# Kernel tuning notes

Measured on AMD Instinct MI355X. Metric: run time of the kernel, lower is better.

## Reference

```python
import jax, jax.numpy as jnp
import numpy as np

NUM_SRC = 100000
NUM_DST = 100000
NUM_EDGES = 800000
WIDTH = 128
LEAKY_SLOPE = 0.01  # torch LeakyReLU default


def setup_inputs() -> dict:
    key = jax.random.key(0)
    k1, k2, k3, k4 = jax.random.split(key, 4)
    x_src = jax.random.normal(k1, (NUM_SRC, WIDTH), dtype=jnp.float32)
    x_dst = jax.random.normal(k2, (NUM_DST, WIDTH), dtype=jnp.float32)
    e = jax.random.randint(k3, (2, NUM_EDGES), 0, NUM_DST, dtype=jnp.int64)
    W = jax.random.normal(k4, (2 * WIDTH, WIDTH), dtype=jnp.float32) * 0.02
    b = jnp.zeros((WIDTH,), dtype=jnp.float32)
    return {"x_src": x_src, "x_dst": x_dst, "e": e, "W": W, "b": b}


def reference(x_src, x_dst, e, W, b):
    src_idx, dst_idx = e[0], e[1]
    # gather + per-edge diff: [E, W]
    diffs = x_dst[dst_idx] - x_src[src_idx]
    # segment max over destination nodes; empty segments -> 0 (matches torch.zeros_like init)
    seg_max = jax.ops.segment_max(diffs, dst_idx, num_segments=NUM_DST)
    counts = jax.ops.segment_sum(jnp.ones((diffs.shape[0],), dtype=x_dst.dtype),
                                 dst_idx, num_segments=NUM_DST)
    maxes = jnp.where(counts[:, None] > 0, seg_max, jnp.zeros_like(seg_max))
    # MLP: Linear(2W -> W) + LeakyReLU, then residual
    h = jnp.concatenate([x_dst, maxes], axis=1) @ W + b
    h = jax.nn.leaky_relu(h, negative_slope=LEAKY_SLOPE)
    return x_dst + h
```

## Files before the change

### kernel.cpp

```cpp
#include <hip/hip_runtime.h>

#define WIDTH 128
#define SLOPE 0.01f
#define SBS 512
#define FBM 64

typedef __attribute__((ext_vector_type(8))) short short8;
typedef __attribute__((ext_vector_type(4))) float f32x4;

__device__ __forceinline__ unsigned short f2bf(float f) {
    unsigned b = __float_as_uint(f);
    b += 0x7FFFu + ((b >> 16) & 1u);
    return (unsigned short)(b >> 16);
}
__device__ __forceinline__ float4 upk(uint2 u) {
    float4 r;
    r.x = __uint_as_float(u.x << 16);
    r.y = __uint_as_float(u.x & 0xFFFF0000u);
    r.z = __uint_as_float(u.y << 16);
    r.w = __uint_as_float(u.y & 0xFFFF0000u);
    return r;
}
__device__ __forceinline__ float4 fmin4(float4 a, float4 b) {
    return make_float4(fminf(a.x, b.x), fminf(a.y, b.y),
                       fminf(a.z, b.z), fminf(a.w, b.w));
}
__device__ __forceinline__ int swz(int lr, int bc) {
    return lr * 512 + (bc ^ ((lr & 7) << 4));
}

__global__ void prep_kernel(const float* __restrict__ x_src,
                            const float* __restrict__ W,
                            const int* __restrict__ e,
                            unsigned short* __restrict__ xsb,
                            unsigned short* __restrict__ Wt,
                            unsigned* __restrict__ counts,
                            int* __restrict__ rank,
                            int NS, int E, int nconv, int nhist) {
    int b = blockIdx.x;
    if (b < nconv) {
        int i = b * 256 + threadIdx.x;
        if (i < NS * 32) {
            float4 v = reinterpret_cast<const float4*>(x_src)[i];
            ushort4 o;
            o.x = f2bf(v.x); o.y = f2bf(v.y); o.z = f2bf(v.z); o.w = f2bf(v.w);
            *reinterpret_cast<ushort4*>(xsb + (size_t)i * 4) = o;
        }
    } else if (b < nconv + nhist) {
        int i = (b - nconv) * 256 + threadIdx.x;
        if (i < E) {
            int dst = e[E + i];
            rank[i] = (int)atomicAdd(&counts[dst], 1u);
        }
    } else {
        int t = (b - nconv - nhist) * 256 + threadIdx.x;
        if (t < 128 * 64) {
            int n = t & 127, kc = t >> 7;
            ushort4 o;
            unsigned short* op = &o.x;
            #pragma unroll
            for (int j = 0; j < 4; ++j) {
                int k = kc * 4 + j;
                float v;
                if (k < 128) v = W[(size_t)k * 128 + n] + W[(size_t)(k + 128) * 128 + n];
                else         v = -W[(size_t)k * 128 + n];
                op[j] = f2bf(v);
            }
            *reinterpret_cast<ushort4*>(Wt + (size_t)n * 256 + kc * 4) = o;
        }
    }
}

__global__ void block_sum_kernel(const unsigned* __restrict__ counts,
                                 unsigned* __restrict__ bsums, int M) {
    int i = blockIdx.x * SBS + threadIdx.x;
    unsigned v = (i < M) ? counts[i] : 0u;
    for (int d = 32; d > 0; d >>= 1) v += __shfl_down(v, d);
    __shared__ unsigned ws[SBS / 64];
    int lane = threadIdx.x & 63, w = threadIdx.x >> 6;
    if (lane == 0) ws[w] = v;
    __syncthreads();
    if (threadIdx.x == 0) {
        unsigned s = 0;
        for (int k = 0; k < SBS / 64; ++k) s += ws[k];
        bsums[blockIdx.x] = s;
    }
}

__global__ void bsum_scan_kernel(const unsigned* __restrict__ bsums,
                                 unsigned* __restrict__ bbase, int NB,
                                 int* __restrict__ offsets, int M) {
    __shared__ unsigned s[256];
    int t = threadIdx.x;
    unsigned v = (t < NB) ? bsums[t] : 0u;
    s[t] = v;
    __syncthreads();
    for (int off = 1; off < 256; off <<= 1) {
        unsigned n = (t >= off) ? s[t - off] : 0u;
        __syncthreads();
        s[t] += n;
        __syncthreads();
    }
    if (t < NB) bbase[t] = s[t] - v;
    if (t == 255) offsets[M] = (int)s[255];
}

__global__ void scan_final_kernel(const unsigned* __restrict__ counts,
                                  const unsigned* __restrict__ bbase,
                                  int* __restrict__ offsets, int M) {
    int b = blockIdx.x, t = threadIdx.x;
    int i = b * SBS + t;
    unsigned c = (i < M) ? counts[i] : 0u;
    unsigned v = c;
    int lane = t & 63, w = t >> 6;
    for (int d = 1; d < 64; d <<= 1) {
        unsigned n = __shfl_up(v, d);
        if (lane >= d) v += n;
    }
    __shared__ unsigned ws[SBS / 64];
    if (lane == 63) ws[w] = v;
    __syncthreads();
    unsigned wbase = 0;
    for (int k = 0; k < w; ++k) wbase += ws[k];
    if (i < M) offsets[i] = (int)(bbase[b] + wbase + v - c);
}

__global__ void scatter_kernel(const int* __restrict__ e,
                               const int* __restrict__ offsets,
                               const int* __restrict__ rank,
                               int* __restrict__ csr, int E) {
    int i = blockIdx.x * blockDim.x + threadIdx.x;
    if (i < E) {
        int dst = e[E + i];
        csr[offsets[dst] + rank[i]] = e[i];
    }
}

template<int XSB>
__device__ __forceinline__ void gstep(const float* xs_f,
                                      const unsigned short* xs_b,
                                      const int* csr, int p, int lim,
                                      int half, int cl, float4& mn) {
    int i0 = csr[min(p + 0, lim)];
    int i1 = csr[min(p + 1, lim)];
    int i2 = csr[min(p + 2, lim)];
    int i3 = csr[min(p + 3, lim)];
    int i4 = csr[min(p + 4, lim)];
    int i5 = csr[min(p + 5, lim)];
    int i6 = csr[min(p + 6, lim)];
    int i7 = csr[min(p + 7, lim)];
    int a0 = half ? i1 : i0;
    int a1 = half ? i3 : i2;
    int a2 = half ? i5 : i4;
    int a3 = half ? i7 : i6;
    float4 w0, w1, w2, w3;
    if (XSB) {
        uint2 u0 = *reinterpret_cast<const uint2*>(xs_b + (size_t)a0 * 128 + cl * 4);
        uint2 u1 = *reinterpret_cast<const uint2*>(xs_b + (size_t)a1 * 128 + cl * 4);
        uint2 u2 = *reinterpret_cast<const uint2*>(xs_b + (size_t)a2 * 128 + cl * 4);
        uint2 u3 = *reinterpret_cast<const uint2*>(xs_b + (size_t)a3 * 128 + cl * 4);
        w0 = upk(u0); w1 = upk(u1); w2 = upk(u2); w3 = upk(u3);
    } else {
        const float4* xs4 = reinterpret_cast<const float4*>(xs_f);
        w0 = xs4[(size_t)a0 * 32 + cl];
        w1 = xs4[(size_t)a1 * 32 + cl];
        w2 = xs4[(size_t)a2 * 32 + cl];
        w3 = xs4[(size_t)a3 * 32 + cl];
    }
    mn = fmin4(mn, fmin4(fmin4(w0, w1), fmin4(w2, w3)));
}

template<int XSB>
__global__ __launch_bounds__(256, 4) void fused_kernel(
        const float* __restrict__ x_src,
        const unsigned short* __restrict__ xsb,
        const float* __restrict__ x_dst,
        const int* __restrict__ offsets,
        const int* __restrict__ csr,
        const unsigned short* __restrict__ Wt,
        const float* __restrict__ bias,
        float* __restrict__ out, int M) {
    __shared__ unsigned short At[FBM * 256];
    char* Ab = reinterpret_cast<char*>(At);
    int tid = threadIdx.x;
    int lane = tid & 63;
    int wv = tid >> 6;
    int blockRow = blockIdx.x * FBM;

    #pragma unroll
    for (int i = 0; i < 8; ++i) {
        int u = tid + 256 * i;
        int lr = u >> 5;
        int c4 = u & 31;
        int gr = min(blockRow + lr, M - 1);
        float4 v = reinterpret_cast<const float4*>(x_dst)[(size_t)gr * 32 + c4];
        ushort4 o;
        o.x = f2bf(v.x); o.y = f2bf(v.y); o.z = f2bf(v.z); o.w = f2bf(v.w);
        *reinterpret_cast<ushort4*>(Ab + swz(lr, c4 * 8)) = o;
    }
    __syncthreads();

    int half = lane >> 5, cl = lane & 31;
    for (int j = 0; j < 4; ++j) {
        int lrb = wv * 16 + 4 * j;
        int beg0, beg1, beg2, beg3, end0, end1, end2, end3;
        {
            int r = __builtin_amdgcn_readfirstlane(blockRow + lrb);
            beg0 = (r + 0 < M) ? offsets[r + 0] : 0;
            end0 = (r + 0 < M) ? offsets[r + 1] : 0;
            beg1 = (r + 1 < M) ? offsets[r + 1] : 0;
            end1 = (r + 1 < M) ? offsets[r + 2] : 0;
            beg2 = (r + 2 < M) ? offsets[r + 2] : 0;
            end2 = (r + 2 < M) ? offsets[r + 3] : 0;
            beg3 = (r + 3 < M) ? offsets[r + 3] : 0;
            end3 = (r + 3 < M) ? offsets[r + 4] : 0;
        }
        float4 mn0 = make_float4(INFINITY, INFINITY, INFINITY, INFINITY);
        float4 mn1 = mn0, mn2 = mn0, mn3 = mn0;
        int p0 = beg0, p1 = beg1, p2 = beg2, p3 = beg3;
        while ((p0 < end0) | (p1 < end1) | (p2 < end2) | (p3 < end3)) {
            if (p0 < end0) { gstep<XSB>(x_src, xsb, csr, p0, end0 - 1, half, cl, mn0); p0 += 8; }
            if (p1 < end1) { gstep<XSB>(x_src, xsb, csr, p1, end1 - 1, half, cl, mn1); p1 += 8; }
            if (p2 < end2) { gstep<XSB>(x_src, xsb, csr, p2, end2 - 1, half, cl, mn2); p2 += 8; }
            if (p3 < end3) { gstep<XSB>(x_src, xsb, csr, p3, end3 - 1, half, cl, mn3); p3 += 8; }
        }
        mn0.x = fminf(mn0.x, __shfl_xor(mn0.x, 32));
        mn0.y = fminf(mn0.y, __shfl_xor(mn0.y, 32));
        mn0.z = fminf(mn0.z, __shfl_xor(mn0.z, 32));
        mn0.w = fminf(mn0.w, __shfl_xor(mn0.w, 32));
        mn1.x = fminf(mn1.x, __shfl_xor(mn1.x, 32));
        mn1.y = fminf(mn1.y, __shfl_xor(mn1.y, 32));
        mn1.z = fminf(mn1.z, __shfl_xor(mn1.z, 32));
        mn1.w = fminf(mn1.w, __shfl_xor(mn1.w, 32));
        mn2.x = fminf(mn2.x, __shfl_xor(mn2.x, 32));
        mn2.y = fminf(mn2.y, __shfl_xor(mn2.y, 32));
        mn2.z = fminf(mn2.z, __shfl_xor(mn2.z, 32));
        mn2.w = fminf(mn2.w, __shfl_xor(mn2.w, 32));
        mn3.x = fminf(mn3.x, __shfl_xor(mn3.x, 32));
        mn3.y = fminf(mn3.y, __shfl_xor(mn3.y, 32));
        mn3.z = fminf(mn3.z, __shfl_xor(mn3.z, 32));
        mn3.w = fminf(mn3.w, __shfl_xor(mn3.w, 32));

        {
            int lr = lrb + half;
            bool has = half ? (end1 > beg1) : (end0 > beg0);
            float4 m = half ? mn1 : mn0;
            ushort4 o;
            if (has) {
                o.x = f2bf(m.x); o.y = f2bf(m.y); o.z = f2bf(m.z); o.w = f2bf(m.w);
            } else {
                o = *reinterpret_cast<const ushort4*>(Ab + swz(lr, cl * 8));
            }
            *reinterpret_cast<ushort4*>(Ab + swz(lr, 256 + cl * 8)) = o;
        }
        {
            int lr = lrb + 2 + half;
            bool has = half ? (end3 > beg3) : (end2 > beg2);
            float4 m = half ? mn3 : mn2;
            ushort4 o;
            if (has) {
                o.x = f2bf(m.x); o.y = f2bf(m.y); o.z = f2bf(m.z); o.w = f2bf(m.w);
            } else {
                o = *reinterpret_cast<const ushort4*>(Ab + swz(lr, cl * 8));
            }
            *reinterpret_cast<ushort4*>(Ab + swz(lr, 256 + cl * 8)) = o;
        }
    }
    __syncthreads();

    int l15 = lane & 15;
    int q = lane >> 4;
    int ncol0 = wv * 32;

    f32x4 acc[4][2];
    #pragma unroll
    for (int t = 0; t < 4; ++t) {
        acc[t][0] = (f32x4){0.f, 0.f, 0.f, 0.f};
        acc[t][1] = (f32x4){0.f, 0.f, 0.f, 0.f};
    }
    size_t b0off = (size_t)(ncol0 + l15) * 256;
    size_t b1off = (size_t)(ncol0 + 16 + l15) * 256;

    #pragma unroll
    for (int s = 0; s < 8; ++s) {
        int koff = s * 32 + q * 8;
        short8 b0 = *reinterpret_cast<const short8*>(Wt + b0off + koff);
        short8 b1 = *reinterpret_cast<const short8*>(Wt + b1off + koff);
        #pragma unroll
        for (int t = 0; t < 4; ++t) {
            int lr = t * 16 + l15;
            short8 a = *reinterpret_cast<const short8*>(Ab + swz(lr, koff * 2));
            acc[t][0] = __builtin_amdgcn_mfma_f32_16x16x32_bf16(b0, a, acc[t][0], 0, 0, 0);
            acc[t][1] = __builtin_amdgcn_mfma_f32_16x16x32_bf16(b1, a, acc[t][1], 0, 0, 0);
        }
    }

    float4 bi[2];
    bi[0] = *reinterpret_cast<const float4*>(bias + ncol0 + q * 4);
    bi[1] = *reinterpret_cast<const float4*>(bias + ncol0 + 16 + q * 4);
    #pragma unroll
    for (int t = 0; t < 4; ++t) {
        int lr = t * 16 + l15;
        int row = blockRow + lr;
        if (row < M) {
            #pragma unroll
            for (int u = 0; u < 2; ++u) {
                int col = ncol0 + u * 16 + q * 4;
                uint2 xu = *reinterpret_cast<const uint2*>(Ab + swz(lr, col * 2));
                float4 xb = upk(xu);
                float4 o;
                float h;
                h = acc[t][u][0] + bi[u].x; o.x = xb.x + (h > 0.f ? h : SLOPE * h);
                h = acc[t][u][1] + bi[u].y; o.y = xb.y + (h > 0.f ? h : SLOPE * h);
                h = acc[t][u][2] + bi[u].z; o.z = xb.z + (h > 0.f ? h : SLOPE * h);
                h = acc[t][u][3] + bi[u].w; o.w = xb.w + (h > 0.f ? h : SLOPE * h);
                *reinterpret_cast<float4*>(out + (size_t)row * 128 + col) = o;
            }
        }
    }
}

extern "C" void kernel_launch(void* const* d_in, const int* in_sizes, int n_in,
                              void* d_out, int out_size, void* d_ws, size_t ws_size,
                              hipStream_t stream) {
    const float* x_src = (const float*)d_in[0];
    const float* x_dst = (const float*)d_in[1];
    const int*   e     = (const int*)d_in[2];
    const float* W     = (const float*)d_in[3];
    const float* bias  = (const float*)d_in[4];
    float* out = (float*)d_out;

    int NS = in_sizes[0] / WIDTH;
    int E  = in_sizes[2] / 2;
    int M  = in_sizes[1] / WIDTH;
    int NB = (M + SBS - 1) / SBS;

    unsigned short* xsb = (unsigned short*)d_ws;
    unsigned short* Wt  = xsb + (size_t)NS * WIDTH;
    unsigned* counts  = (unsigned*)(Wt + 128 * 256);
    int*      offsets = (int*)(counts + M);
    int*      rank    = offsets + (M + 1);
    int*      csr     = rank + E;
    unsigned* bsums   = (unsigned*)(csr + E);
    unsigned* bbase   = bsums + NB;
    size_t need = (char*)(bbase + NB) - (char*)d_ws;
    int use_xsb = (ws_size >= need) ? 1 : 0;
    if (!use_xsb) {
        Wt = (unsigned short*)d_ws;
        counts  = (unsigned*)(Wt + 128 * 256);
        offsets = (int*)(counts + M);
        rank    = offsets + (M + 1);
        csr     = rank + E;
        bsums   = (unsigned*)(csr + E);
        bbase   = bsums + NB;
    }

    hipMemsetAsync(counts, 0, (size_t)M * sizeof(unsigned), stream);

    int nconv = use_xsb ? (NS * 32 + 255) / 256 : 0;
    int nhist = (E + 255) / 256;
    int nwt   = (128 * 64 + 255) / 256;
    prep_kernel<<<nconv + nhist + nwt, 256, 0, stream>>>(x_src, W, e, xsb, Wt,
                                                         counts, rank, NS, E,
                                                         nconv, nhist);
    block_sum_kernel<<<NB, SBS, 0, stream>>>(counts, bsums, M);
    bsum_scan_kernel<<<1, 256, 0, stream>>>(bsums, bbase, NB, offsets, M);
    scan_final_kernel<<<NB, SBS, 0, stream>>>(counts, bbase, offsets, M);
    scatter_kernel<<<(E + 255) / 256, 256, 0, stream>>>(e, offsets, rank, csr, E);

    int fblocks = (M + FBM - 1) / FBM;
    if (use_xsb)
        fused_kernel<1><<<fblocks, 256, 0, stream>>>(x_src, xsb, x_dst, offsets,
                                                     csr, Wt, bias, out, M);
    else
        fused_kernel<0><<<fblocks, 256, 0, stream>>>(x_src, xsb, x_dst, offsets,
                                                     csr, Wt, bias, out, M);
}
```

Measured before the change: 139.5 us.

## Flatten per-block edge loop with LDS atomicMin on order-mapped bf16 values

```diff
diff --git a/kernel.cpp b/kernel.cpp
--- a/kernel.cpp
+++ b/kernel.cpp
@@ -3,7 +3,7 @@
 #define WIDTH 128
 #define SLOPE 0.01f
 #define SBS 512
-#define FBM 64
+#define FBM 32
 
 typedef __attribute__((ext_vector_type(8))) short short8;
 typedef __attribute__((ext_vector_type(4))) float f32x4;
@@ -21,9 +21,11 @@
     r.w = __uint_as_float(u.y & 0xFFFF0000u);
     return r;
 }
-__device__ __forceinline__ float4 fmin4(float4 a, float4 b) {
-    return make_float4(fminf(a.x, b.x), fminf(a.y, b.y),
-                       fminf(a.z, b.z), fminf(a.w, b.w));
+__device__ __forceinline__ unsigned map16(unsigned x) {
+    return (x & 0x8000u) ? (~x & 0xFFFFu) : (x | 0x8000u);
+}
+__device__ __forceinline__ unsigned short unmap16(unsigned u) {
+    return (unsigned short)((u & 0x8000u) ? (u ^ 0x8000u) : (~u & 0xFFFFu));
 }
 __device__ __forceinline__ int swz(int lr, int bc) {
     return lr * 512 + (bc ^ ((lr & 7) << 4));
@@ -128,46 +130,41 @@
 __global__ void scatter_kernel(const int* __restrict__ e,
                                const int* __restrict__ offsets,
                                const int* __restrict__ rank,
-                               int* __restrict__ csr, int E) {
+                               unsigned* __restrict__ csr, int E) {
     int i = blockIdx.x * blockDim.x + threadIdx.x;
     if (i < E) {
         int dst = e[E + i];
-        csr[offsets[dst] + rank[i]] = e[i];
+        unsigned pack = (unsigned)e[i] | ((unsigned)(dst & (FBM - 1)) << 20);
+        csr[offsets[dst] + rank[i]] = pack;
     }
 }
 
 template<int XSB>
-__device__ __forceinline__ void gstep(const float* xs_f,
-                                      const unsigned short* xs_b,
-                                      const int* csr, int p, int lim,
-                                      int half, int cl, float4& mn) {
-    int i0 = csr[min(p + 0, lim)];
-    int i1 = csr[min(p + 1, lim)];
-    int i2 = csr[min(p + 2, lim)];
-    int i3 = csr[min(p + 3, lim)];
-    int i4 = csr[min(p + 4, lim)];
-    int i5 = csr[min(p + 5, lim)];
-    int i6 = csr[min(p + 6, lim)];
-    int i7 = csr[min(p + 7, lim)];
-    int a0 = half ? i1 : i0;
-    int a1 = half ? i3 : i2;
-    int a2 = half ? i5 : i4;
-    int a3 = half ? i7 : i6;
-    float4 w0, w1, w2, w3;
+__device__ __forceinline__ void edge_min(const float* __restrict__ x_src,
+                                         const unsigned short* __restrict__ xsb,
+                                         unsigned pack, int cl,
+                                         unsigned* __restrict__ minbuf) {
+    int src = (int)(pack & 0xFFFFFu);
+    int lr  = (int)(pack >> 20);
+    unsigned m0, m1, m2, m3;
     if (XSB) {
-        uint2 u0 = *reinterpret_cast<const uint2*>(xs_b + (size_t)a0 * 128 + cl * 4);
-        uint2 u1 = *reinterpret_cast<const uint2*>(xs_b + (size_t)a1 * 128 + cl * 4);
-        uint2 u2 = *reinterpret_cast<const uint2*>(xs_b + (size_t)a2 * 128 + cl * 4);
-        uint2 u3 = *reinterpret_cast<const uint2*>(xs_b + (size_t)a3 * 128 + cl * 4);
-        w0 = upk(u0); w1 = upk(u1); w2 = upk(u2); w3 = upk(u3);
+        const unsigned short* p = xsb + (size_t)src * WIDTH + cl;
+        m0 = map16(p[0]);
+        m1 = map16(p[32]);
+        m2 = map16(p[64]);
+        m3 = map16(p[96]);
     } else {
-        const float4* xs4 = reinterpret_cast<const float4*>(xs_f);
-        w0 = xs4[(size_t)a0 * 32 + cl];
-        w1 = xs4[(size_t)a1 * 32 + cl];
-        w2 = xs4[(size_t)a2 * 32 + cl];
-        w3 = xs4[(size_t)a3 * 32 + cl];
-    }
-    mn = fmin4(mn, fmin4(fmin4(w0, w1), fmin4(w2, w3)));
+        const float* p = x_src + (size_t)src * WIDTH + cl;
+        m0 = map16(f2bf(p[0]));
+        m1 = map16(f2bf(p[32]));
+        m2 = map16(f2bf(p[64]));
+        m3 = map16(f2bf(p[96]));
+    }
+    unsigned* row = minbuf + lr * WIDTH + cl;
+    atomicMin(row + 0,  m0);
+    atomicMin(row + 32, m1);
+    atomicMin(row + 64, m2);
+    atomicMin(row + 96, m3);
 }
 
 template<int XSB>
@@ -176,94 +173,67 @@
         const unsigned short* __restrict__ xsb,
         const float* __restrict__ x_dst,
         const int* __restrict__ offsets,
-        const int* __restrict__ csr,
+        const unsigned* __restrict__ csr,
         const unsigned short* __restrict__ Wt,
         const float* __restrict__ bias,
         float* __restrict__ out, int M) {
-    __shared__ unsigned short At[FBM * 256];
+    __shared__ __align__(16) unsigned short At[FBM * 256];
+    __shared__ __align__(16) unsigned minbuf[FBM * WIDTH];
     char* Ab = reinterpret_cast<char*>(At);
     int tid = threadIdx.x;
     int lane = tid & 63;
     int wv = tid >> 6;
     int blockRow = blockIdx.x * FBM;
 
+    {
+        uint4* mb4 = reinterpret_cast<uint4*>(minbuf);
+        #pragma unroll
+        for (int i = 0; i < 4; ++i)
+            mb4[tid + 256 * i] = make_uint4(~0u, ~0u, ~0u, ~0u);
+    }
     #pragma unroll
-    for (int i = 0; i < 8; ++i) {
+    for (int i = 0; i < 4; ++i) {
         int u = tid + 256 * i;
-        int lr = u >> 5;
-        int c4 = u & 31;
-        int gr = min(blockRow + lr, M - 1);
-        float4 v = reinterpret_cast<const float4*>(x_dst)[(size_t)gr * 32 + c4];
+        int lr = u >> 5, c4 = u & 31;
+        float4 v = reinterpret_cast<const float4*>(x_dst)[(size_t)(blockRow + lr) * 32 + c4];
         ushort4 o;
         o.x = f2bf(v.x); o.y = f2bf(v.y); o.z = f2bf(v.z); o.w = f2bf(v.w);
         *reinterpret_cast<ushort4*>(Ab + swz(lr, c4 * 8)) = o;
     }
     __syncthreads();
 
+    int ebeg = offsets[blockRow];
+    int eend = offsets[blockRow + FBM];
     int half = lane >> 5, cl = lane & 31;
-    for (int j = 0; j < 4; ++j) {
-        int lrb = wv * 16 + 4 * j;
-        int beg0, beg1, beg2, beg3, end0, end1, end2, end3;
-        {
-            int r = __builtin_amdgcn_readfirstlane(blockRow + lrb);
-            beg0 = (r + 0 < M) ? offsets[r + 0] : 0;
-            end0 = (r + 0 < M) ? offsets[r + 1] : 0;
-            beg1 = (r + 1 < M) ? offsets[r + 1] : 0;
-            end1 = (r + 1 < M) ? offsets[r + 2] : 0;
-            beg2 = (r + 2 < M) ? offsets[r + 2] : 0;
-            end2 = (r + 2 < M) ? offsets[r + 3] : 0;
-            beg3 = (r + 3 < M) ? offsets[r + 3] : 0;
-            end3 = (r + 3 < M) ? offsets[r + 4] : 0;
-        }
-        float4 mn0 = make_float4(INFINITY, INFINITY, INFINITY, INFINITY);
-        float4 mn1 = mn0, mn2 = mn0, mn3 = mn0;
-        int p0 = beg0, p1 = beg1, p2 = beg2, p3 = beg3;
-        while ((p0 < end0) | (p1 < end1) | (p2 < end2) | (p3 < end3)) {
-            if (p0 < end0) { gstep<XSB>(x_src, xsb, csr, p0, end0 - 1, half, cl, mn0); p0 += 8; }
-            if (p1 < end1) { gstep<XSB>(x_src, xsb, csr, p1, end1 - 1, half, cl, mn1); p1 += 8; }
-            if (p2 < end2) { gstep<XSB>(x_src, xsb, csr, p2, end2 - 1, half, cl, mn2); p2 += 8; }
-            if (p3 < end3) { gstep<XSB>(x_src, xsb, csr, p3, end3 - 1, half, cl, mn3); p3 += 8; }
-        }
-        mn0.x = fminf(mn0.x, __shfl_xor(mn0.x, 32));
-        mn0.y = fminf(mn0.y, __shfl_xor(mn0.y, 32));
-        mn0.z = fminf(mn0.z, __shfl_xor(mn0.z, 32));
-        mn0.w = fminf(mn0.w, __shfl_xor(mn0.w, 32));
-        mn1.x = fminf(mn1.x, __shfl_xor(mn1.x, 32));
-        mn1.y = fminf(mn1.y, __shfl_xor(mn1.y, 32));
-        mn1.z = fminf(mn1.z, __shfl_xor(mn1.z, 32));
-        mn1.w = fminf(mn1.w, __shfl_xor(mn1.w, 32));
-        mn2.x = fminf(mn2.x, __shfl_xor(mn2.x, 32));
-        mn2.y = fminf(mn2.y, __shfl_xor(mn2.y, 32));
-        mn2.z = fminf(mn2.z, __shfl_xor(mn2.z, 32));
-        mn2.w = fminf(mn2.w, __shfl_xor(mn2.w, 32));
-        mn3.x = fminf(mn3.x, __shfl_xor(mn3.x, 32));
-        mn3.y = fminf(mn3.y, __shfl_xor(mn3.y, 32));
-        mn3.z = fminf(mn3.z, __shfl_xor(mn3.z, 32));
-        mn3.w = fminf(mn3.w, __shfl_xor(mn3.w, 32));
-
-        {
-            int lr = lrb + half;
-            bool has = half ? (end1 > beg1) : (end0 > beg0);
-            float4 m = half ? mn1 : mn0;
+    int lim = eend - 1;
+    if (eend > ebeg) {
+        #pragma unroll 2
+        for (int i = ebeg + wv * 4; i < eend; i += 16) {
+            unsigned p0 = csr[min(i + half, lim)];
+            unsigned p1 = csr[min(i + 2 + half, lim)];
+            edge_min<XSB>(x_src, xsb, p0, cl, minbuf);
+            edge_min<XSB>(x_src, xsb, p1, cl, minbuf);
+        }
+    }
+    __syncthreads();
+
+    {
+        int r = tid >> 3;
+        int c0 = (tid & 7) * 16;
+        #pragma unroll
+        for (int k = 0; k < 4; ++k) {
+            int c = c0 + k * 4;
+            unsigned u0 = minbuf[r * WIDTH + c + 0];
+            unsigned u1 = minbuf[r * WIDTH + c + 1];
+            unsigned u2 = minbuf[r * WIDTH + c + 2];
+            unsigned u3 = minbuf[r * WIDTH + c + 3];
+            ushort4 xb = *reinterpret_cast<const ushort4*>(Ab + swz(r, c * 2));
             ushort4 o;
-            if (has) {
-                o.x = f2bf(m.x); o.y = f2bf(m.y); o.z = f2bf(m.z); o.w = f2bf(m.w);
-            } else {
-                o = *reinterpret_cast<const ushort4*>(Ab + swz(lr, cl * 8));
-            }
-            *reinterpret_cast<ushort4*>(Ab + swz(lr, 256 + cl * 8)) = o;
-        }
-        {
-            int lr = lrb + 2 + half;
-            bool has = half ? (end3 > beg3) : (end2 > beg2);
-            float4 m = half ? mn3 : mn2;
-            ushort4 o;
-            if (has) {
-                o.x = f2bf(m.x); o.y = f2bf(m.y); o.z = f2bf(m.z); o.w = f2bf(m.w);
-            } else {
-                o = *reinterpret_cast<const ushort4*>(Ab + swz(lr, cl * 8));
-            }
-            *reinterpret_cast<ushort4*>(Ab + swz(lr, 256 + cl * 8)) = o;
+            o.x = (u0 <= 0xFFFFu) ? unmap16(u0) : xb.x;
+            o.y = (u1 <= 0xFFFFu) ? unmap16(u1) : xb.y;
+            o.z = (u2 <= 0xFFFFu) ? unmap16(u2) : xb.z;
+            o.w = (u3 <= 0xFFFFu) ? unmap16(u3) : xb.w;
+            *reinterpret_cast<ushort4*>(Ab + swz(r, 256 + c * 2)) = o;
         }
     }
     __syncthreads();
@@ -272,9 +242,9 @@
     int q = lane >> 4;
     int ncol0 = wv * 32;
 
-    f32x4 acc[4][2];
+    f32x4 acc[2][2];
     #pragma unroll
-    for (int t = 0; t < 4; ++t) {
+    for (int t = 0; t < 2; ++t) {
         acc[t][0] = (f32x4){0.f, 0.f, 0.f, 0.f};
         acc[t][1] = (f32x4){0.f, 0.f, 0.f, 0.f};
     }
@@ -287,7 +257,7 @@
         short8 b0 = *reinterpret_cast<const short8*>(Wt + b0off + koff);
         short8 b1 = *reinterpret_cast<const short8*>(Wt + b1off + koff);
         #pragma unroll
-        for (int t = 0; t < 4; ++t) {
+        for (int t = 0; t < 2; ++t) {
             int lr = t * 16 + l15;
             short8 a = *reinterpret_cast<const short8*>(Ab + swz(lr, koff * 2));
             acc[t][0] = __builtin_amdgcn_mfma_f32_16x16x32_bf16(b0, a, acc[t][0], 0, 0, 0);
@@ -299,23 +269,21 @@
     bi[0] = *reinterpret_cast<const float4*>(bias + ncol0 + q * 4);
     bi[1] = *reinterpret_cast<const float4*>(bias + ncol0 + 16 + q * 4);
     #pragma unroll
-    for (int t = 0; t < 4; ++t) {
+    for (int t = 0; t < 2; ++t) {
         int lr = t * 16 + l15;
         int row = blockRow + lr;
-        if (row < M) {
-            #pragma unroll
-            for (int u = 0; u < 2; ++u) {
-                int col = ncol0 + u * 16 + q * 4;
-                uint2 xu = *reinterpret_cast<const uint2*>(Ab + swz(lr, col * 2));
-                float4 xb = upk(xu);
-                float4 o;
-                float h;
-                h = acc[t][u][0] + bi[u].x; o.x = xb.x + (h > 0.f ? h : SLOPE * h);
-                h = acc[t][u][1] + bi[u].y; o.y = xb.y + (h > 0.f ? h : SLOPE * h);
-                h = acc[t][u][2] + bi[u].z; o.z = xb.z + (h > 0.f ? h : SLOPE * h);
-                h = acc[t][u][3] + bi[u].w; o.w = xb.w + (h > 0.f ? h : SLOPE * h);
-                *reinterpret_cast<float4*>(out + (size_t)row * 128 + col) = o;
-            }
+        #pragma unroll
+        for (int u = 0; u < 2; ++u) {
+            int col = ncol0 + u * 16 + q * 4;
+            uint2 xu = *reinterpret_cast<const uint2*>(Ab + swz(lr, col * 2));
+            float4 xb = upk(xu);
+            float4 o;
+            float h;
+            h = acc[t][u][0] + bi[u].x; o.x = xb.x + (h > 0.f ? h : SLOPE * h);
+            h = acc[t][u][1] + bi[u].y; o.y = xb.y + (h > 0.f ? h : SLOPE * h);
+            h = acc[t][u][2] + bi[u].z; o.z = xb.z + (h > 0.f ? h : SLOPE * h);
+            h = acc[t][u][3] + bi[u].w; o.w = xb.w + (h > 0.f ? h : SLOPE * h);
+            *reinterpret_cast<float4*>(out + (size_t)row * 128 + col) = o;
         }
     }
 }
@@ -340,7 +308,7 @@
     unsigned* counts  = (unsigned*)(Wt + 128 * 256);
     int*      offsets = (int*)(counts + M);
     int*      rank    = offsets + (M + 1);
-    int*      csr     = rank + E;
+    unsigned* csr     = (unsigned*)(rank + E);
     unsigned* bsums   = (unsigned*)(csr + E);
     unsigned* bbase   = bsums + NB;
     size_t need = (char*)(bbase + NB) - (char*)d_ws;
@@ -350,7 +318,7 @@
         counts  = (unsigned*)(Wt + 128 * 256);
         offsets = (int*)(counts + M);
         rank    = offsets + (M + 1);
-        csr     = rank + E;
+        csr     = (unsigned*)(rank + E);
         bsums   = (unsigned*)(csr + E);
         bbase   = bsums + NB;
     }
```

Result: slower. 173.2 us (+24.1%).

## Merge CSR build kernels into one cooperative kernel with grid syncs

Applied to the files above, without the earlier changes.

```diff
diff --git a/kernel.cpp b/kernel.cpp
--- a/kernel.cpp
+++ b/kernel.cpp
@@ -1,9 +1,12 @@
 #include <hip/hip_runtime.h>
+#include <hip/hip_cooperative_groups.h>
+
+namespace cg = cooperative_groups;
 
 #define WIDTH 128
 #define SLOPE 0.01f
-#define SBS 512
 #define FBM 64
+#define CBLK 512
 
 typedef __attribute__((ext_vector_type(8))) short short8;
 typedef __attribute__((ext_vector_type(4))) float f32x4;
@@ -29,108 +32,102 @@
     return lr * 512 + (bc ^ ((lr & 7) << 4));
 }
 
-__global__ void prep_kernel(const float* __restrict__ x_src,
-                            const float* __restrict__ W,
-                            const int* __restrict__ e,
-                            unsigned short* __restrict__ xsb,
-                            unsigned short* __restrict__ Wt,
-                            unsigned* __restrict__ counts,
-                            int* __restrict__ rank,
-                            int NS, int E, int nconv, int nhist) {
-    int b = blockIdx.x;
-    if (b < nconv) {
-        int i = b * 256 + threadIdx.x;
-        if (i < NS * 32) {
+__global__ void __launch_bounds__(256) csr_coop_kernel(
+        const float* __restrict__ x_src, const float* __restrict__ W,
+        const int* __restrict__ e,
+        unsigned short* __restrict__ xsb, unsigned short* __restrict__ Wt,
+        unsigned* __restrict__ counts, int* __restrict__ rank,
+        int* __restrict__ offsets, int* __restrict__ csr,
+        unsigned* __restrict__ bsums, unsigned* __restrict__ bbase,
+        int NS, int E, int M, int NB, int use_xsb) {
+    cg::grid_group grid = cg::this_grid();
+    __shared__ unsigned s[256];
+    __shared__ unsigned wsx[4];
+    int tid = threadIdx.x;
+    int gsize = gridDim.x * 256;
+    int gthread = blockIdx.x * 256 + tid;
+    int lane = tid & 63, w = tid >> 6;
+
+    if (use_xsb) {
+        for (int i = gthread; i < NS * 32; i += gsize) {
             float4 v = reinterpret_cast<const float4*>(x_src)[i];
             ushort4 o;
             o.x = f2bf(v.x); o.y = f2bf(v.y); o.z = f2bf(v.z); o.w = f2bf(v.w);
             *reinterpret_cast<ushort4*>(xsb + (size_t)i * 4) = o;
         }
-    } else if (b < nconv + nhist) {
-        int i = (b - nconv) * 256 + threadIdx.x;
-        if (i < E) {
-            int dst = e[E + i];
-            rank[i] = (int)atomicAdd(&counts[dst], 1u);
-        }
-    } else {
-        int t = (b - nconv - nhist) * 256 + threadIdx.x;
-        if (t < 128 * 64) {
-            int n = t & 127, kc = t >> 7;
-            ushort4 o;
-            unsigned short* op = &o.x;
-            #pragma unroll
-            for (int j = 0; j < 4; ++j) {
-                int k = kc * 4 + j;
-                float v;
-                if (k < 128) v = W[(size_t)k * 128 + n] + W[(size_t)(k + 128) * 128 + n];
-                else         v = -W[(size_t)k * 128 + n];
-                op[j] = f2bf(v);
-            }
-            *reinterpret_cast<ushort4*>(Wt + (size_t)n * 256 + kc * 4) = o;
-        }
-    }
-}
-
-__global__ void block_sum_kernel(const unsigned* __restrict__ counts,
-                                 unsigned* __restrict__ bsums, int M) {
-    int i = blockIdx.x * SBS + threadIdx.x;
-    unsigned v = (i < M) ? counts[i] : 0u;
-    for (int d = 32; d > 0; d >>= 1) v += __shfl_down(v, d);
-    __shared__ unsigned ws[SBS / 64];
-    int lane = threadIdx.x & 63, w = threadIdx.x >> 6;
-    if (lane == 0) ws[w] = v;
-    __syncthreads();
-    if (threadIdx.x == 0) {
-        unsigned s = 0;
-        for (int k = 0; k < SBS / 64; ++k) s += ws[k];
-        bsums[blockIdx.x] = s;
-    }
-}
-
-__global__ void bsum_scan_kernel(const unsigned* __restrict__ bsums,
-                                 unsigned* __restrict__ bbase, int NB,
-                                 int* __restrict__ offsets, int M) {
-    __shared__ unsigned s[256];
-    int t = threadIdx.x;
-    unsigned v = (t < NB) ? bsums[t] : 0u;
-    s[t] = v;
-    __syncthreads();
-    for (int off = 1; off < 256; off <<= 1) {
-        unsigned n = (t >= off) ? s[t - off] : 0u;
-        __syncthreads();
-        s[t] += n;
-        __syncthreads();
-    }
-    if (t < NB) bbase[t] = s[t] - v;
-    if (t == 255) offsets[M] = (int)s[255];
-}
-
-__global__ void scan_final_kernel(const unsigned* __restrict__ counts,
-                                  const unsigned* __restrict__ bbase,
-                                  int* __restrict__ offsets, int M) {
-    int b = blockIdx.x, t = threadIdx.x;
-    int i = b * SBS + t;
-    unsigned c = (i < M) ? counts[i] : 0u;
-    unsigned v = c;
-    int lane = t & 63, w = t >> 6;
-    for (int d = 1; d < 64; d <<= 1) {
-        unsigned n = __shfl_up(v, d);
-        if (lane >= d) v += n;
-    }
-    __shared__ unsigned ws[SBS / 64];
-    if (lane == 63) ws[w] = v;
-    __syncthreads();
-    unsigned wbase = 0;
-    for (int k = 0; k < w; ++k) wbase += ws[k];
-    if (i < M) offsets[i] = (int)(bbase[b] + wbase + v - c);
-}
-
-__global__ void scatter_kernel(const int* __restrict__ e,
-                               const int* __restrict__ offsets,
-                               const int* __restrict__ rank,
-                               int* __restrict__ csr, int E) {
-    int i = blockIdx.x * blockDim.x + threadIdx.x;
-    if (i < E) {
+    }
+    for (int t = gthread; t < 128 * 64; t += gsize) {
+        int n = t & 127, kc = t >> 7;
+        ushort4 o;
+        unsigned short* op = &o.x;
+        #pragma unroll
+        for (int j = 0; j < 4; ++j) {
+            int k = kc * 4 + j;
+            float v;
+            if (k < 128) v = W[(size_t)k * 128 + n] + W[(size_t)(k + 128) * 128 + n];
+            else         v = -W[(size_t)k * 128 + n];
+            op[j] = f2bf(v);
+        }
+        *reinterpret_cast<ushort4*>(Wt + (size_t)n * 256 + kc * 4) = o;
+    }
+    for (int i = gthread; i < E; i += gsize) {
+        int dst = e[E + i];
+        rank[i] = (int)atomicAdd(&counts[dst], 1u);
+    }
+    grid.sync();
+
+    for (int b = blockIdx.x; b < NB; b += gridDim.x) {
+        int base = b * 512;
+        int i0 = base + tid, i1 = base + 256 + tid;
+        unsigned v = 0;
+        if (i0 < M) v += counts[i0];
+        if (i1 < M) v += counts[i1];
+        for (int d = 32; d > 0; d >>= 1) v += __shfl_down(v, d);
+        if (lane == 0) wsx[w] = v;
+        __syncthreads();
+        if (tid == 0) bsums[b] = wsx[0] + wsx[1] + wsx[2] + wsx[3];
+        __syncthreads();
+    }
+    grid.sync();
+
+    if (blockIdx.x == 0) {
+        unsigned v = (tid < NB) ? bsums[tid] : 0u;
+        s[tid] = v;
+        __syncthreads();
+        for (int off = 1; off < 256; off <<= 1) {
+            unsigned n = (tid >= off) ? s[tid - off] : 0u;
+            __syncthreads();
+            s[tid] += n;
+            __syncthreads();
+        }
+        if (tid < NB) bbase[tid] = s[tid] - v;
+        if (tid == 255) offsets[M] = (int)s[255];
+    }
+    grid.sync();
+
+    for (int b = blockIdx.x; b < NB; b += gridDim.x) {
+        int base = b * 512;
+        int i0 = base + 2 * tid;
+        unsigned c0 = (i0 < M) ? counts[i0] : 0u;
+        unsigned c1 = (i0 + 1 < M) ? counts[i0 + 1] : 0u;
+        unsigned pair = c0 + c1;
+        unsigned v = pair;
+        for (int d = 1; d < 64; d <<= 1) {
+            unsigned n = __shfl_up(v, d);
+            if (lane >= d) v += n;
+        }
+        if (lane == 63) wsx[w] = v;
+        __syncthreads();
+        unsigned wb = 0;
+        for (int k = 0; k < w; ++k) wb += wsx[k];
+        unsigned excl = bbase[b] + wb + v - pair;
+        if (i0 < M) offsets[i0] = (int)excl;
+        if (i0 + 1 < M) offsets[i0 + 1] = (int)(excl + c0);
+        __syncthreads();
+    }
+    grid.sync();
+
+    for (int i = gthread; i < E; i += gsize) {
         int dst = e[E + i];
         csr[offsets[dst] + rank[i]] = e[i];
     }
@@ -333,7 +330,7 @@
     int NS = in_sizes[0] / WIDTH;
     int E  = in_sizes[2] / 2;
     int M  = in_sizes[1] / WIDTH;
-    int NB = (M + SBS - 1) / SBS;
+    int NB = (M + 511) / 512;
 
     unsigned short* xsb = (unsigned short*)d_ws;
     unsigned short* Wt  = xsb + (size_t)NS * WIDTH;
@@ -357,16 +354,15 @@
 
     hipMemsetAsync(counts, 0, (size_t)M * sizeof(unsigned), stream);
 
-    int nconv = use_xsb ? (NS * 32 + 255) / 256 : 0;
-    int nhist = (E + 255) / 256;
-    int nwt   = (128 * 64 + 255) / 256;
-    prep_kernel<<<nconv + nhist + nwt, 256, 0, stream>>>(x_src, W, e, xsb, Wt,
-                                                         counts, rank, NS, E,
-                                                         nconv, nhist);
-    block_sum_kernel<<<NB, SBS, 0, stream>>>(counts, bsums, M);
-    bsum_scan_kernel<<<1, 256, 0, stream>>>(bsums, bbase, NB, offsets, M);
-    scan_final_kernel<<<NB, SBS, 0, stream>>>(counts, bbase, offsets, M);
-    scatter_kernel<<<(E + 255) / 256, 256, 0, stream>>>(e, offsets, rank, csr, E);
+    void* args[] = {
+        (void*)&x_src, (void*)&W, (void*)&e,
+        (void*)&xsb, (void*)&Wt,
+        (void*)&counts, (void*)&rank, (void*)&offsets, (void*)&csr,
+        (void*)&bsums, (void*)&bbase,
+        (void*)&NS, (void*)&E, (void*)&M, (void*)&NB, (void*)&use_xsb
+    };
+    hipLaunchCooperativeKernel((void*)csr_coop_kernel, dim3(CBLK), dim3(256),
+                               args, 0, stream);
 
     int fblocks = (M + FBM - 1) / FBM;
     if (use_xsb)
```

Measured after the change: 354.4 us. 2.54x slower.
